# Optimization experiments

Hardware: AMD Instinct MI355X
Metric: run time of the kernel (lower is better)

Reference implementation:

```python
import jax, jax.numpy as jnp
import numpy as np

B, S, E, H, D = 4, 2048, 1024, 16, 64


def setup_inputs() -> dict:
    key = jax.random.key(0)
    ks = jax.random.split(key, 6)
    scale_in = 1.0 / np.sqrt(E)
    return {
        "x": jax.random.normal(ks[0], (B, S, E), dtype=jnp.float32),
        "Wq": jax.random.normal(ks[1], (H, E, D), dtype=jnp.float32) * scale_in,
        "bq": jnp.zeros((H, D), dtype=jnp.float32),
        "Wk": jax.random.normal(ks[2], (H, E, D), dtype=jnp.float32) * scale_in,
        "bk": jnp.zeros((H, D), dtype=jnp.float32),
        "Wv": jax.random.normal(ks[3], (H, E, D), dtype=jnp.float32) * scale_in,
        "bv": jnp.zeros((H, D), dtype=jnp.float32),
        "Wo": jax.random.normal(ks[4], (H * D, E), dtype=jnp.float32) * (1.0 / np.sqrt(H * D)),
        "bo": jnp.zeros((E,), dtype=jnp.float32),
    }


def reference(x, Wq, bq, Wk, bk, Wv, bv, Wo, bo):
    # Per-head Q/K/V projections, batched over heads: [B,S,E] x [H,E,D] -> [B,H,S,D]
    q = jnp.einsum("bse,hed->bhsd", x, Wq) + bq[None, :, None, :]
    k = jnp.einsum("bse,hed->bhsd", x, Wk) + bk[None, :, None, :]
    v = jnp.einsum("bse,hed->bhsd", x, Wv) + bv[None, :, None, :]

    d = q.shape[-1]
    scores = jnp.einsum("bhqd,bhkd->bhqk", q, k) / jnp.sqrt(jnp.asarray(d, q.dtype))
    # Causal mask (registered tril buffer of size max_seq_len in HeadAttention)
    seq = scores.shape[-1]
    causal = jnp.tril(jnp.ones((seq, seq), dtype=bool))
    scores = jnp.where(causal[None, None, :, :], scores, jnp.asarray(-1e9, scores.dtype))
    attn = jax.nn.softmax(scores, axis=-1)
    out = jnp.einsum("bhqk,bhkd->bhqd", attn, v)  # [B,H,S,D]

    # Concat heads: [B,S,H*D], then output projection (dropout is identity in eval)
    out = out.transpose(0, 2, 1, 3).reshape(out.shape[0], out.shape[2], -1)
    return out @ Wo + bo
```

## Files before the change

kernel.cpp:

```cpp
#include <hip/hip_runtime.h>

typedef __bf16 bf16x8 __attribute__((ext_vector_type(8)));
typedef __bf16 bf16x4 __attribute__((ext_vector_type(4)));
typedef float  f32x4  __attribute__((ext_vector_type(4)));

#define B_    4
#define S_    2048
#define E_    1024
#define H_    16
#define D_    64
#define MROWS (B_*S_)
#define HD3   3072

#define SCORE_SCALE 0.18033688011112043f

__device__ __forceinline__ void load_lds16(const void* g, void* l) {
  __builtin_amdgcn_global_load_lds((__attribute__((address_space(1))) void*)g,
                                   (__attribute__((address_space(3))) void*)l,
                                   16, 0, 0);
}

__device__ __forceinline__ f32x4 mfma16(bf16x8 a, bf16x8 b, f32x4 c) {
  return __builtin_amdgcn_mfma_f32_16x16x32_bf16(a, b, c, 0, 0, 0);
}

__device__ __forceinline__ int swz(int row, int dchunk) {
  return row * 64 + ((dchunk ^ (row & 7)) * 8);
}


__global__ void cvt_x(const float4* __restrict__ x, __bf16* __restrict__ y) {
  int id = blockIdx.x * 256 + threadIdx.x;
  float4 v = x[id];
  bf16x4 o = { (__bf16)v.x, (__bf16)v.y, (__bf16)v.z, (__bf16)v.w };
  *(bf16x4*)(y + 4 * (size_t)id) = o;
}

__global__ void pack_w(const float* __restrict__ Wq, const float* __restrict__ Wk,
                       const float* __restrict__ Wv, const float* __restrict__ bq,
                       const float* __restrict__ bk, const float* __restrict__ bv,
                       __bf16* __restrict__ Wt, float* __restrict__ bqkv) {
  __shared__ float t[64][65];
  int bid = blockIdx.x;
  int e0 = (bid & 15) * 64;
  int h  = (bid >> 4) & 15;
  int p  = bid >> 8;
  const float* W    = (p == 0) ? Wq : (p == 1) ? Wk : Wv;
  const float* bsrc = (p == 0) ? bq : (p == 1) ? bk : bv;
  int tx = threadIdx.x & 63;
  int ty = threadIdx.x >> 6;
#pragma unroll
  for (int r = 0; r < 16; ++r) {
    int eL = ty + r * 4;
    t[eL][tx] = W[((size_t)h * 1024 + (e0 + eL)) * 64 + tx];
  }
  __syncthreads();
#pragma unroll
  for (int r = 0; r < 16; ++r) {
    int d = ty + r * 4;
    Wt[((size_t)(p * 1024 + h * 64 + d)) * 1024 + e0 + tx] = (__bf16)t[tx][d];
  }
  if ((bid & 15) == 0 && threadIdx.x < 64)
    bqkv[p * 1024 + h * 64 + threadIdx.x] = bsrc[h * 64 + threadIdx.x];
}

__global__ void pack_wo(const float* __restrict__ Wo, __bf16* __restrict__ Wot) {
  __shared__ float t[64][65];
  int hd0 = (blockIdx.x >> 4) * 64;
  int e0  = (blockIdx.x & 15) * 64;
  int tx = threadIdx.x & 63;
  int ty = threadIdx.x >> 6;
#pragma unroll
  for (int r = 0; r < 16; ++r) {
    int hdL = ty + r * 4;
    t[hdL][tx] = Wo[(size_t)(hd0 + hdL) * 1024 + e0 + tx];
  }
  __syncthreads();
#pragma unroll
  for (int r = 0; r < 16; ++r) {
    int eL = ty + r * 4;
    Wot[(size_t)(e0 + eL) * 1024 + hd0 + tx] = (__bf16)t[tx][eL];
  }
}

__global__ void vt_pack(const __bf16* __restrict__ QKV, __bf16* __restrict__ VT) {
  __shared__ __attribute__((aligned(16))) __bf16 t[64 * 80];
  int bx = blockIdx.x;
  int st = bx & 31, bh = bx >> 5;
  int b = bh >> 4, h = bh & 15;
  int s0 = st * 64;
  const __bf16* src = QKV + ((size_t)(b * S_ + s0)) * HD3 + 2048 + h * 64;
  int tid = threadIdx.x;
#pragma unroll
  for (int p = 0; p < 2; ++p) {
    int g = tid + p * 256;
    int s = g >> 3, ch = g & 7;
    bf16x8 v = *(const bf16x8*)(src + (size_t)s * HD3 + ch * 8);
    *(bf16x8*)&t[s * 80 + ch * 8] = v;
  }
  __syncthreads();
#pragma unroll
  for (int p = 0; p < 2; ++p) {
    int g = tid + p * 256;
    int d = g >> 3, sc = g & 7;
    bf16x8 v;
#pragma unroll
    for (int u = 0; u < 8; ++u) v[u] = t[(sc * 8 + u) * 80 + d];
    *(bf16x8*)&VT[((size_t)(bh * 64 + d)) * 2048 + s0 + sc * 8] = v;
  }
}


template <int STORE_BF16, int QSCALE>
__global__ __launch_bounds__(256) void gemm_bt(const __bf16* __restrict__ A,
                                               const __bf16* __restrict__ Bt,
                                               const float* __restrict__ bias,
                                               void* __restrict__ Cout,
                                               int M, int N, int K) {
  __shared__ __attribute__((aligned(16))) __bf16 As[128 * 32];
  __shared__ __attribute__((aligned(16))) __bf16 Bs[128 * 32];
  int tid = threadIdx.x, wave = tid >> 6, lane = tid & 63;
  int quad = lane >> 4, cc = lane & 15;
  int nb = N >> 7;
  int bm = (int)blockIdx.x / nb, bn = (int)blockIdx.x % nb;
  const __bf16* Abase = A + (size_t)bm * 128 * K;
  const __bf16* Bbase = Bt + (size_t)bn * 128 * K;
  int wr = (wave >> 1) * 64, wc = (wave & 1) * 64;
  f32x4 acc[4][4];
#pragma unroll
  for (int i = 0; i < 4; ++i)
#pragma unroll
    for (int j = 0; j < 4; ++j) acc[i][j] = (f32x4){0.f, 0.f, 0.f, 0.f};

  for (int k0 = 0; k0 < K; k0 += 32) {
    __syncthreads();
#pragma unroll
    for (int p = 0; p < 2; ++p) {
      int cidx = tid + p * 256;
      int row = cidx >> 2, col8 = (cidx & 3) * 8;
      load_lds16(Abase + (size_t)row * K + k0 + col8, &As[cidx * 8]);
      load_lds16(Bbase + (size_t)row * K + k0 + col8, &Bs[cidx * 8]);
    }
    __syncthreads();
    bf16x8 af[4], bf[4];
#pragma unroll
    for (int i = 0; i < 4; ++i) af[i] = *(const bf16x8*)&As[(wr + i * 16 + cc) * 32 + quad * 8];
#pragma unroll
    for (int j = 0; j < 4; ++j) bf[j] = *(const bf16x8*)&Bs[(wc + j * 16 + cc) * 32 + quad * 8];
#pragma unroll
    for (int i = 0; i < 4; ++i)
#pragma unroll
      for (int j = 0; j < 4; ++j) acc[i][j] = mfma16(af[i], bf[j], acc[i][j]);
  }
#pragma unroll
  for (int j = 0; j < 4; ++j) {
    int col = bn * 128 + wc + j * 16 + cc;
    float bv = bias[col];
    float sc = (QSCALE && col < 1024) ? SCORE_SCALE : 1.0f;
#pragma unroll
    for (int i = 0; i < 4; ++i) {
      int row0 = bm * 128 + wr + i * 16 + quad * 4;
#pragma unroll
      for (int r = 0; r < 4; ++r) {
        float v = (acc[i][j][r] + bv) * sc;
        if (STORE_BF16) ((__bf16*)Cout)[(size_t)(row0 + r) * N + col] = (__bf16)v;
        else            ((float*)Cout)[(size_t)(row0 + r) * N + col] = v;
      }
    }
  }
}


__global__ __launch_bounds__(256, 2) void attn(const __bf16* __restrict__ QKV,
                                               const __bf16* __restrict__ VT,
                                               __bf16* __restrict__ O) {
  int bx = blockIdx.x;
  int bh = bx & 63;
  int qt = 15 - (bx >> 6);
  int h  = bh & 15;
  int b  = bh >> 4;
  int q0 = qt * 128;
  int tid = threadIdx.x, wave = tid >> 6, lane = tid & 63;
  int quad = lane >> 4, c = lane & 15;

  __shared__ __attribute__((aligned(16))) __bf16 smem[32768];
  __bf16* Qs = smem;
  __bf16* Ks = smem + 8192;
  __bf16* Vs = smem + 16384;
  __bf16* Ps = smem + 24576 + wave * 2048;

  const __bf16* Qbase = QKV + (size_t)(b * S_ + q0) * HD3 + h * 64;
  const __bf16* Vbase = VT + (size_t)bh * (64 * 2048);
#pragma unroll
  for (int p = 0; p < 4; ++p) {
    int g = tid + p * 256;
    int row = g >> 3, pch = g & 7;
    load_lds16(Qbase + (size_t)row * HD3 + (pch ^ (row & 7)) * 8, &Qs[g * 8]);
  }
  {
    const __bf16* Kb = QKV + (size_t)(b * S_) * HD3 + 1024 + h * 64;
#pragma unroll
    for (int p = 0; p < 2; ++p) {
      int g = tid + p * 256;
      int row = g >> 3, pch = g & 7;
      load_lds16(Kb + (size_t)row * HD3 + (pch ^ (row & 7)) * 8, &Ks[g * 8]);
      load_lds16(Vbase + (size_t)row * 2048 + (pch ^ (row & 7)) * 8, &Vs[g * 8]);
    }
  }
  __syncthreads();

  bf16x8 qf[2][2];
#pragma unroll
  for (int i = 0; i < 2; ++i)
#pragma unroll
    for (int kk = 0; kk < 2; ++kk)
      qf[i][kk] = *(const bf16x8*)&Qs[swz(wave * 32 + i * 16 + c, kk * 4 + quad)];

  const __bf16 one_b = (__bf16)1.0f;
  bf16x8 ones = { one_b, one_b, one_b, one_b, one_b, one_b, one_b, one_b };

  f32x4 acc_o[2][4], acc_l[2];
#pragma unroll
  for (int i = 0; i < 2; ++i) {
    acc_l[i] = (f32x4){0.f, 0.f, 0.f, 0.f};
#pragma unroll
    for (int j = 0; j < 4; ++j) acc_o[i][j] = (f32x4){0.f, 0.f, 0.f, 0.f};
  }

  int ntiles = qt * 2 + 2;
  for (int t = 0; t < ntiles; ++t) {
    int cur = t & 1;
    if (t + 1 < ntiles) {
      int kv1 = (t + 1) * 64;
      const __bf16* Kb = QKV + (size_t)(b * S_ + kv1) * HD3 + 1024 + h * 64;
      const __bf16* Vb = Vbase + kv1;
      __bf16* Kd = Ks + (cur ^ 1) * 4096;
      __bf16* Vd = Vs + (cur ^ 1) * 4096;
#pragma unroll
      for (int p = 0; p < 2; ++p) {
        int g = tid + p * 256;
        int row = g >> 3, pch = g & 7;
        load_lds16(Kb + (size_t)row * HD3 + (pch ^ (row & 7)) * 8, &Kd[g * 8]);
        load_lds16(Vb + (size_t)row * 2048 + (pch ^ (row & 7)) * 8, &Vd[g * 8]);
      }
    }

    const __bf16* Kc = Ks + cur * 4096;
    const __bf16* Vc = Vs + cur * 4096;

    f32x4 acc_s[2][4];
#pragma unroll
    for (int i = 0; i < 2; ++i)
#pragma unroll
      for (int j = 0; j < 4; ++j) acc_s[i][j] = (f32x4){0.f, 0.f, 0.f, 0.f};
    bf16x8 kf[4][2];
#pragma unroll
    for (int j = 0; j < 4; ++j)
#pragma unroll
      for (int kk = 0; kk < 2; ++kk)
        kf[j][kk] = *(const bf16x8*)&Kc[swz(j * 16 + c, kk * 4 + quad)];
#pragma unroll
    for (int i = 0; i < 2; ++i)
#pragma unroll
      for (int j = 0; j < 4; ++j)
#pragma unroll
        for (int kk = 0; kk < 2; ++kk)
          acc_s[i][j] = mfma16(qf[i][kk], kf[j][kk], acc_s[i][j]);

    bool domask = (t >= ntiles - 2);
    int kv0 = t * 64;
#pragma unroll
    for (int i = 0; i < 2; ++i)
#pragma unroll
      for (int j = 0; j < 4; ++j)
#pragma unroll
        for (int r = 0; r < 4; ++r) {
          float p = __builtin_amdgcn_exp2f(acc_s[i][j][r]);
          if (domask) {
            int row = q0 + wave * 32 + i * 16 + quad * 4 + r;
            int col = kv0 + j * 16 + c;
            p = (col > row) ? 0.f : p;
          }
          int q = i * 16 + quad * 4 + r;
          int dch = j * 2 + (c >> 3);
          Ps[q * 64 + ((dch ^ (q & 7)) * 8) + (c & 7)] = (__bf16)p;
        }

    bf16x8 pf[2][2], vf[4][2];
#pragma unroll
    for (int i = 0; i < 2; ++i)
#pragma unroll
      for (int kk = 0; kk < 2; ++kk)
        pf[i][kk] = *(const bf16x8*)&Ps[swz(i * 16 + c, kk * 4 + quad)];
#pragma unroll
    for (int j = 0; j < 4; ++j)
#pragma unroll
      for (int kk = 0; kk < 2; ++kk)
        vf[j][kk] = *(const bf16x8*)&Vc[swz(j * 16 + c, kk * 4 + quad)];
#pragma unroll
    for (int i = 0; i < 2; ++i) {
#pragma unroll
      for (int j = 0; j < 4; ++j)
#pragma unroll
        for (int kk = 0; kk < 2; ++kk)
          acc_o[i][j] = mfma16(pf[i][kk], vf[j][kk], acc_o[i][j]);
      acc_l[i] = mfma16(pf[i][0], ones, acc_l[i]);
      acc_l[i] = mfma16(pf[i][1], ones, acc_l[i]);
    }

    __syncthreads();
  }

  __bf16* Obase = O + (size_t)(b * S_ + q0) * 1024 + h * 64;
#pragma unroll
  for (int i = 0; i < 2; ++i)
#pragma unroll
    for (int r = 0; r < 4; ++r) {
      float rl = 1.0f / acc_l[i][r];
      int row = wave * 32 + i * 16 + quad * 4 + r;
#pragma unroll
      for (int j = 0; j < 4; ++j)
        Obase[(size_t)row * 1024 + j * 16 + c] = (__bf16)(acc_o[i][j][r] * rl);
    }
}


extern "C" void kernel_launch(void* const* d_in, const int* in_sizes, int n_in,
                              void* d_out, int out_size, void* d_ws, size_t ws_size,
                              hipStream_t stream) {
  (void)in_sizes; (void)n_in; (void)out_size; (void)ws_size;
  const float* x  = (const float*)d_in[0];
  const float* Wq = (const float*)d_in[1];
  const float* bq = (const float*)d_in[2];
  const float* Wk = (const float*)d_in[3];
  const float* bk = (const float*)d_in[4];
  const float* Wv = (const float*)d_in[5];
  const float* bv = (const float*)d_in[6];
  const float* Wo = (const float*)d_in[7];
  const float* bo = (const float*)d_in[8];

  char* w = (char*)d_ws;
  __bf16* xb   = (__bf16*)(w);
  __bf16* Wt   = (__bf16*)(w + (16ull << 20));
  __bf16* Wot  = (__bf16*)(w + (22ull << 20));
  float*  bqkv = (float*) (w + (24ull << 20));
  __bf16* QKVb = (__bf16*)(w + (25ull << 20));
  __bf16* Ob   = (__bf16*)(w + (73ull << 20));
  __bf16* VT   = (__bf16*)(w + (89ull << 20));

  cvt_x  <<<8192, 256, 0, stream>>>((const float4*)x, xb);
  pack_w <<<768,  256, 0, stream>>>(Wq, Wk, Wv, bq, bk, bv, Wt, bqkv);
  pack_wo<<<256,  256, 0, stream>>>(Wo, Wot);
  gemm_bt<1,1><<<dim3((MROWS / 128) * (3072 / 128)), 256, 0, stream>>>(xb, Wt, bqkv, (void*)QKVb, MROWS, 3072, 1024);
  vt_pack<<<2048, 256, 0, stream>>>(QKVb, VT);
  attn   <<<1024, 256, 0, stream>>>(QKVb, VT, Ob);
  gemm_bt<0,0><<<dim3((MROWS / 128) * (1024 / 128)), 256, 0, stream>>>(Ob, Wot, bo, d_out, MROWS, 1024, 1024);
}
```

Before: 280.8 us.

## Merge prep kernels, widen GEMM K-tile with swizzle, alias P buffer, transpose scores

```diff
diff --git a/kernel.cpp b/kernel.cpp
--- a/kernel.cpp
+++ b/kernel.cpp
@@ -29,57 +29,58 @@
 }
 
 
-__global__ void cvt_x(const float4* __restrict__ x, __bf16* __restrict__ y) {
-  int id = blockIdx.x * 256 + threadIdx.x;
-  float4 v = x[id];
-  bf16x4 o = { (__bf16)v.x, (__bf16)v.y, (__bf16)v.z, (__bf16)v.w };
-  *(bf16x4*)(y + 4 * (size_t)id) = o;
-}
-
-__global__ void pack_w(const float* __restrict__ Wq, const float* __restrict__ Wk,
-                       const float* __restrict__ Wv, const float* __restrict__ bq,
-                       const float* __restrict__ bk, const float* __restrict__ bv,
-                       __bf16* __restrict__ Wt, float* __restrict__ bqkv) {
+__global__ void prep(const float4* __restrict__ x, const float* __restrict__ Wq,
+                     const float* __restrict__ Wk, const float* __restrict__ Wv,
+                     const float* __restrict__ bq, const float* __restrict__ bk,
+                     const float* __restrict__ bv, const float* __restrict__ Wo,
+                     __bf16* __restrict__ xb, __bf16* __restrict__ Wt,
+                     float* __restrict__ bqkv, __bf16* __restrict__ Wot) {
   __shared__ float t[64][65];
   int bid = blockIdx.x;
-  int e0 = (bid & 15) * 64;
-  int h  = (bid >> 4) & 15;
-  int p  = bid >> 8;
-  const float* W    = (p == 0) ? Wq : (p == 1) ? Wk : Wv;
-  const float* bsrc = (p == 0) ? bq : (p == 1) ? bk : bv;
+  if (bid < 8192) {
+    int id = bid * 256 + threadIdx.x;
+    float4 v = x[id];
+    bf16x4 o = { (__bf16)v.x, (__bf16)v.y, (__bf16)v.z, (__bf16)v.w };
+    *(bf16x4*)(xb + 4 * (size_t)id) = o;
+    return;
+  }
   int tx = threadIdx.x & 63;
   int ty = threadIdx.x >> 6;
-#pragma unroll
-  for (int r = 0; r < 16; ++r) {
-    int eL = ty + r * 4;
-    t[eL][tx] = W[((size_t)h * 1024 + (e0 + eL)) * 64 + tx];
-  }
-  __syncthreads();
-#pragma unroll
-  for (int r = 0; r < 16; ++r) {
-    int d = ty + r * 4;
-    Wt[((size_t)(p * 1024 + h * 64 + d)) * 1024 + e0 + tx] = (__bf16)t[tx][d];
-  }
-  if ((bid & 15) == 0 && threadIdx.x < 64)
-    bqkv[p * 1024 + h * 64 + threadIdx.x] = bsrc[h * 64 + threadIdx.x];
-}
-
-__global__ void pack_wo(const float* __restrict__ Wo, __bf16* __restrict__ Wot) {
-  __shared__ float t[64][65];
-  int hd0 = (blockIdx.x >> 4) * 64;
-  int e0  = (blockIdx.x & 15) * 64;
-  int tx = threadIdx.x & 63;
-  int ty = threadIdx.x >> 6;
-#pragma unroll
-  for (int r = 0; r < 16; ++r) {
-    int hdL = ty + r * 4;
-    t[hdL][tx] = Wo[(size_t)(hd0 + hdL) * 1024 + e0 + tx];
-  }
-  __syncthreads();
-#pragma unroll
-  for (int r = 0; r < 16; ++r) {
-    int eL = ty + r * 4;
-    Wot[(size_t)(e0 + eL) * 1024 + hd0 + tx] = (__bf16)t[tx][eL];
+  if (bid < 8960) {
+    int b2 = bid - 8192;
+    int e0 = (b2 & 15) * 64;
+    int h  = (b2 >> 4) & 15;
+    int p  = b2 >> 8;
+    const float* W    = (p == 0) ? Wq : (p == 1) ? Wk : Wv;
+    const float* bsrc = (p == 0) ? bq : (p == 1) ? bk : bv;
+#pragma unroll
+    for (int r = 0; r < 16; ++r) {
+      int eL = ty + r * 4;
+      t[eL][tx] = W[((size_t)h * 1024 + (e0 + eL)) * 64 + tx];
+    }
+    __syncthreads();
+#pragma unroll
+    for (int r = 0; r < 16; ++r) {
+      int d = ty + r * 4;
+      Wt[((size_t)(p * 1024 + h * 64 + d)) * 1024 + e0 + tx] = (__bf16)t[tx][d];
+    }
+    if ((b2 & 15) == 0 && threadIdx.x < 64)
+      bqkv[p * 1024 + h * 64 + threadIdx.x] = bsrc[h * 64 + threadIdx.x];
+  } else {
+    int b2 = bid - 8960;
+    int hd0 = (b2 >> 4) * 64;
+    int e0  = (b2 & 15) * 64;
+#pragma unroll
+    for (int r = 0; r < 16; ++r) {
+      int hdL = ty + r * 4;
+      t[hdL][tx] = Wo[(size_t)(hd0 + hdL) * 1024 + e0 + tx];
+    }
+    __syncthreads();
+#pragma unroll
+    for (int r = 0; r < 16; ++r) {
+      int eL = ty + r * 4;
+      Wot[(size_t)(e0 + eL) * 1024 + hd0 + tx] = (__bf16)t[tx][eL];
+    }
   }
 }
 
@@ -117,8 +118,8 @@
                                                const float* __restrict__ bias,
                                                void* __restrict__ Cout,
                                                int M, int N, int K) {
-  __shared__ __attribute__((aligned(16))) __bf16 As[128 * 32];
-  __shared__ __attribute__((aligned(16))) __bf16 Bs[128 * 32];
+  __shared__ __attribute__((aligned(16))) __bf16 As[128 * 64];
+  __shared__ __attribute__((aligned(16))) __bf16 Bs[128 * 64];
   int tid = threadIdx.x, wave = tid >> 6, lane = tid & 63;
   int quad = lane >> 4, cc = lane & 15;
   int nb = N >> 7;
@@ -132,25 +133,29 @@
 #pragma unroll
     for (int j = 0; j < 4; ++j) acc[i][j] = (f32x4){0.f, 0.f, 0.f, 0.f};
 
-  for (int k0 = 0; k0 < K; k0 += 32) {
-    __syncthreads();
-#pragma unroll
-    for (int p = 0; p < 2; ++p) {
-      int cidx = tid + p * 256;
-      int row = cidx >> 2, col8 = (cidx & 3) * 8;
-      load_lds16(Abase + (size_t)row * K + k0 + col8, &As[cidx * 8]);
-      load_lds16(Bbase + (size_t)row * K + k0 + col8, &Bs[cidx * 8]);
-    }
-    __syncthreads();
-    bf16x8 af[4], bf[4];
-#pragma unroll
-    for (int i = 0; i < 4; ++i) af[i] = *(const bf16x8*)&As[(wr + i * 16 + cc) * 32 + quad * 8];
-#pragma unroll
-    for (int j = 0; j < 4; ++j) bf[j] = *(const bf16x8*)&Bs[(wc + j * 16 + cc) * 32 + quad * 8];
-#pragma unroll
-    for (int i = 0; i < 4; ++i)
-#pragma unroll
-      for (int j = 0; j < 4; ++j) acc[i][j] = mfma16(af[i], bf[j], acc[i][j]);
+  for (int k0 = 0; k0 < K; k0 += 64) {
+    __syncthreads();
+#pragma unroll
+    for (int p = 0; p < 4; ++p) {
+      int g = tid + p * 256;
+      int row = g >> 3, pch = g & 7;
+      int gcol = k0 + ((pch ^ (row & 7)) * 8);
+      load_lds16(Abase + (size_t)row * K + gcol, &As[g * 8]);
+      load_lds16(Bbase + (size_t)row * K + gcol, &Bs[g * 8]);
+    }
+    __syncthreads();
+#pragma unroll
+    for (int kk = 0; kk < 2; ++kk) {
+      bf16x8 af[4], bf[4];
+#pragma unroll
+      for (int i = 0; i < 4; ++i) af[i] = *(const bf16x8*)&As[swz(wr + i * 16 + cc, kk * 4 + quad)];
+#pragma unroll
+      for (int j = 0; j < 4; ++j) bf[j] = *(const bf16x8*)&Bs[swz(wc + j * 16 + cc, kk * 4 + quad)];
+#pragma unroll
+      for (int i = 0; i < 4; ++i)
+#pragma unroll
+        for (int j = 0; j < 4; ++j) acc[i][j] = mfma16(af[i], bf[j], acc[i][j]);
+    }
   }
 #pragma unroll
   for (int j = 0; j < 4; ++j) {
@@ -171,7 +176,7 @@
 }
 
 
-__global__ __launch_bounds__(256, 2) void attn(const __bf16* __restrict__ QKV,
+__global__ __launch_bounds__(256, 3) void attn(const __bf16* __restrict__ QKV,
                                                const __bf16* __restrict__ VT,
                                                __bf16* __restrict__ O) {
   int bx = blockIdx.x;
@@ -183,11 +188,11 @@
   int tid = threadIdx.x, wave = tid >> 6, lane = tid & 63;
   int quad = lane >> 4, c = lane & 15;
 
-  __shared__ __attribute__((aligned(16))) __bf16 smem[32768];
+  __shared__ __attribute__((aligned(16))) __bf16 smem[24576];
   __bf16* Qs = smem;
   __bf16* Ks = smem + 8192;
   __bf16* Vs = smem + 16384;
-  __bf16* Ps = smem + 24576 + wave * 2048;
+  __bf16* Ps = smem + wave * 2048;
 
   const __bf16* Qbase = QKV + (size_t)(b * S_ + q0) * HD3 + h * 64;
   const __bf16* Vbase = VT + (size_t)bh * (64 * 2048);
@@ -248,11 +253,11 @@
     const __bf16* Kc = Ks + cur * 4096;
     const __bf16* Vc = Vs + cur * 4096;
 
-    f32x4 acc_s[2][4];
+    f32x4 acc_t[2][4];
 #pragma unroll
     for (int i = 0; i < 2; ++i)
 #pragma unroll
-      for (int j = 0; j < 4; ++j) acc_s[i][j] = (f32x4){0.f, 0.f, 0.f, 0.f};
+      for (int j = 0; j < 4; ++j) acc_t[i][j] = (f32x4){0.f, 0.f, 0.f, 0.f};
     bf16x8 kf[4][2];
 #pragma unroll
     for (int j = 0; j < 4; ++j)
@@ -265,26 +270,31 @@
       for (int j = 0; j < 4; ++j)
 #pragma unroll
         for (int kk = 0; kk < 2; ++kk)
-          acc_s[i][j] = mfma16(qf[i][kk], kf[j][kk], acc_s[i][j]);
+          acc_t[i][j] = mfma16(kf[j][kk], qf[i][kk], acc_t[i][j]);
 
     bool domask = (t >= ntiles - 2);
     int kv0 = t * 64;
 #pragma unroll
-    for (int i = 0; i < 2; ++i)
-#pragma unroll
-      for (int j = 0; j < 4; ++j)
+    for (int i = 0; i < 2; ++i) {
+      int q_l = i * 16 + c;
+      int q_g = q0 + wave * 32 + q_l;
+#pragma unroll
+      for (int j = 0; j < 4; ++j) {
+        bf16x4 pk;
 #pragma unroll
         for (int r = 0; r < 4; ++r) {
-          float p = __builtin_amdgcn_exp2f(acc_s[i][j][r]);
+          float p = __builtin_amdgcn_exp2f(acc_t[i][j][r]);
           if (domask) {
-            int row = q0 + wave * 32 + i * 16 + quad * 4 + r;
-            int col = kv0 + j * 16 + c;
-            p = (col > row) ? 0.f : p;
+            int kv = kv0 + j * 16 + quad * 4 + r;
+            p = (kv > q_g) ? 0.f : p;
           }
-          int q = i * 16 + quad * 4 + r;
-          int dch = j * 2 + (c >> 3);
-          Ps[q * 64 + ((dch ^ (q & 7)) * 8) + (c & 7)] = (__bf16)p;
+          pk[r] = (__bf16)p;
         }
+        int dch8 = j * 2 + (quad >> 1);
+        int phys = q_l * 64 + ((dch8 ^ (q_l & 7)) * 8) + (quad & 1) * 4;
+        *(bf16x4*)&Ps[phys] = pk;
+      }
+    }
 
     bf16x8 pf[2][2], vf[4][2];
 #pragma unroll
@@ -348,9 +358,8 @@
   __bf16* Ob   = (__bf16*)(w + (73ull << 20));
   __bf16* VT   = (__bf16*)(w + (89ull << 20));
 
-  cvt_x  <<<8192, 256, 0, stream>>>((const float4*)x, xb);
-  pack_w <<<768,  256, 0, stream>>>(Wq, Wk, Wv, bq, bk, bv, Wt, bqkv);
-  pack_wo<<<256,  256, 0, stream>>>(Wo, Wot);
+  prep   <<<9216, 256, 0, stream>>>((const float4*)x, Wq, Wk, Wv, bq, bk, bv, Wo,
+                                    xb, Wt, bqkv, Wot);
   gemm_bt<1,1><<<dim3((MROWS / 128) * (3072 / 128)), 256, 0, stream>>>(xb, Wt, bqkv, (void*)QKVb, MROWS, 3072, 1024);
   vt_pack<<<2048, 256, 0, stream>>>(QKVb, VT);
   attn   <<<1024, 256, 0, stream>>>(QKVb, VT, Ob);
```

Measured after the change: 259.8 us. 7.5% less time.
